# Kernel optimization log

Hardware: AMD Instinct MI355X
Metric: run time of the kernel (lower is better)

The kernel has to match this reference:

```python
import jax, jax.numpy as jnp
import numpy as np


def setup_inputs() -> dict:
    key = jax.random.key(0)
    k1, k2, k3, k4 = jax.random.split(key, 4)
    B, S, E, A = 4, 4096, 1024, 1024
    embedded = jax.random.normal(k1, (B, S, E), dtype=jnp.float32)
    # nn.Linear(E, A, bias=False) weights, stored as [E, A] so y = x @ W
    Wk = jax.random.normal(k2, (E, A), dtype=jnp.float32) * (E ** -0.5)
    Wq = jax.random.normal(k3, (E, A), dtype=jnp.float32) * (E ** -0.5)
    Wv = jax.random.normal(k4, (E, A), dtype=jnp.float32) * (E ** -0.5)
    return {"embedded": embedded, "Wk": Wk, "Wq": Wq, "Wv": Wv}


def reference(embedded, Wk, Wq, Wv):
    # K, Q, V projections: [B, S, A]
    K = embedded @ Wk
    Q = embedded @ Wq
    V = embedded @ Wv
    A = K.shape[-1]
    S = embedded.shape[1]
    # causal scores [B, S, S]
    scores = jnp.einsum("bqa,bka->bqk", Q, K) / jnp.sqrt(jnp.float32(A))
    causal = jnp.tril(jnp.ones((S, S), dtype=bool))
    scores = jnp.where(causal, scores, -jnp.inf)
    probs = jax.nn.softmax(scores, axis=-1)
    out = jnp.einsum("bqk,bka->bqa", probs, V)
    # torch.round(out, decimals=4)
    return jnp.round(out, 4)
```

## Files before the change

kernel.cpp:

```cpp
#include <hip/hip_runtime.h>
#include <hip/hip_fp16.h>

typedef __attribute__((ext_vector_type(4))) float f32x4;
typedef __attribute__((ext_vector_type(8))) short s16x8;
typedef __attribute__((ext_vector_type(4))) short s16x4;
typedef unsigned short u16;
typedef unsigned int u32;

__device__ __forceinline__ u16 f2bf(float f) {
    union { float f; unsigned u; } x; x.f = f;
    return (u16)((x.u + 0x7fffu + ((x.u >> 16) & 1u)) >> 16);
}

__device__ __forceinline__ void ld16(const void* g, void* l) {
    __builtin_amdgcn_global_load_lds(
        (const __attribute__((address_space(1))) unsigned int*)g,
        (__attribute__((address_space(3))) unsigned int*)l, 16, 0, 0);
}

__device__ __forceinline__ void kstep64(const u16* gA, const u16* gB, const u16* gC,
                                        long lda, long ldb,
                                        u16* sA, u16* sB,
                                        int wm, int wn, int lm, int lg,
                                        f32x4 acc0[4][4], f32x4 acc1[4][4])
{
    const int t = threadIdx.x;
    __syncthreads();
#pragma unroll
    for (int p = 0; p < 4; p++) {
        ld16(gA + (long)p * 32 * lda, sA + p * 2048 + t * 8);
        ld16(gB + (long)p * 32 * ldb, sB + p * 2048 + t * 8);
        ld16(gC + (long)p * 32 * ldb, sB + 8192 + p * 2048 + t * 8);
    }
    __syncthreads();

#pragma unroll
    for (int s = 0; s < 2; s++) {
        s16x8 af[4], bf[4], cf[4];
        const int co = (((s * 4 + lg) ^ (lm & 7)) << 3);
#pragma unroll
        for (int i = 0; i < 4; i++) {
            af[i] = *(const s16x8*)&sA[(wm + i * 16 + lm) * 64 + co];
            bf[i] = *(const s16x8*)&sB[(wn + i * 16 + lm) * 64 + co];
            cf[i] = *(const s16x8*)&sB[8192 + (wn + i * 16 + lm) * 64 + co];
        }
#pragma unroll
        for (int i = 0; i < 4; i++)
#pragma unroll
            for (int j = 0; j < 4; j++) {
                acc0[i][j] = __builtin_amdgcn_mfma_f32_16x16x32_bf16(af[i], bf[j], acc0[i][j], 0, 0, 0);
                acc1[i][j] = __builtin_amdgcn_mfma_f32_16x16x32_bf16(af[i], cf[j], acc1[i][j], 0, 0, 0);
            }
    }
}

__device__ __forceinline__ void gemm_core64(const u16* A, long lda,
                                            const u16* B0, const u16* B1, long ldb,
                                            int m0, int kEnd,
                                            f32x4 acc0[4][4], f32x4 acc1[4][4],
                                            u16* sA, u16* sB)
{
    const int t    = threadIdx.x;
    const int lane = t & 63;
    const int wave = t >> 6;
    const int wm   = (wave & 1) << 6;
    const int wn   = (wave >> 1) << 6;
    const int lm   = lane & 15;
    const int lg   = lane >> 4;
    const int sr   = t >> 3;
    const int sc   = (((t & 7) ^ ((t >> 3) & 7)) << 3);
    const u16* gA0 = A + (long)(m0 + sr) * lda + sc;
    const u16* gB0 = B0 + (long)sr * ldb + sc;
    const u16* gC0 = B1 + (long)sr * ldb + sc;

    for (int k0 = 0; k0 < kEnd; k0 += 64)
        kstep64(gA0 + k0, gB0 + k0, gC0 + k0, lda, ldb,
                sA, sB, wm, wn, lm, lg, acc0, acc1);
}

__global__ void convert_x(const float* __restrict__ X, u16* __restrict__ Xb) {
    long idx = ((long)blockIdx.x * 256 + threadIdx.x) * 4;
    f32x4 v = *(const f32x4*)&X[idx];
    s16x4 o;
    o.x = (short)f2bf(v.x); o.y = (short)f2bf(v.y);
    o.z = (short)f2bf(v.z); o.w = (short)f2bf(v.w);
    *(s16x4*)&Xb[idx] = o;
}

__global__ void convert_w(const float* __restrict__ Wk, const float* __restrict__ Wq,
                          const float* __restrict__ Wv,
                          u16* __restrict__ Wkt, u16* __restrict__ Wqt, u16* __restrict__ Wvt) {
    const float* W; u16* O;
    if (blockIdx.y == 0)      { W = Wk; O = Wkt; }
    else if (blockIdx.y == 1) { W = Wq; O = Wqt; }
    else                      { W = Wv; O = Wvt; }
    __shared__ u16 tile[64][65];
    int k0 = (blockIdx.x >> 4) << 6, n0 = (blockIdx.x & 15) << 6;
    int t = threadIdx.x;
    int rr = t >> 4, cc = (t & 15) << 2;
#pragma unroll
    for (int i = 0; i < 4; i++) {
        int row = rr + i * 16;
        f32x4 v = *(const f32x4*)&W[(long)(k0 + row) * 1024 + n0 + cc];
        tile[row][cc + 0] = f2bf(v.x); tile[row][cc + 1] = f2bf(v.y);
        tile[row][cc + 2] = f2bf(v.z); tile[row][cc + 3] = f2bf(v.w);
    }
    __syncthreads();
#pragma unroll
    for (int i = 0; i < 4; i++) {
        int row = rr + i * 16;
        s16x4 pk;
        pk.x = (short)tile[cc + 0][row]; pk.y = (short)tile[cc + 1][row];
        pk.z = (short)tile[cc + 2][row]; pk.w = (short)tile[cc + 3][row];
        *(s16x4*)&O[(long)(n0 + row) * 1024 + k0 + cc] = pk;
    }
}

__device__ __forceinline__ void stage_half64(const u16* gbase, u16* lbase,
                                             int kt, int h, int t) {
    const u16* g = gbase + (long)(h * 128) * 1024 + kt * 64;
    u16* l = lbase + h * 8192 + t * 8;
    ld16(g, l);
    ld16(g + 64 * 1024, l + 4096);
}

__device__ __forceinline__ void read_A8(const u16* sA, int arow, int ih,
                                        int co0, int co1, s16x8 af[4][2]) {
#pragma unroll
    for (int i = 0; i < 4; i++) {
        af[i][0] = *(const s16x8*)&sA[(arow + (ih * 4 + i) * 16) * 64 + co0];
        af[i][1] = *(const s16x8*)&sA[(arow + (ih * 4 + i) * 16) * 64 + co1];
    }
}

__device__ __forceinline__ void read_B4(const u16* sB, int brow, int jp,
                                        int co0, int co1, s16x8 bf[4][2]) {
#pragma unroll
    for (int j = 2 * jp; j < 2 * jp + 2; j++) {
        bf[j][0] = *(const s16x8*)&sB[(brow + j * 16) * 64 + co0];
        bf[j][1] = *(const s16x8*)&sB[(brow + j * 16) * 64 + co1];
    }
}

__device__ __forceinline__ void mfma16q(f32x4 acc[8][4], const s16x8 af[4][2],
                                        const s16x8 bf[4][2], int ih, int jh) {
    __builtin_amdgcn_s_setprio(1);
#pragma unroll
    for (int s = 0; s < 2; s++)
#pragma unroll
        for (int i = 0; i < 4; i++)
#pragma unroll
            for (int j = 0; j < 2; j++)
                acc[ih * 4 + i][jh * 2 + j] = __builtin_amdgcn_mfma_f32_16x16x32_bf16(
                    af[i][s], bf[jh * 2 + j][s], acc[ih * 4 + i][jh * 2 + j], 0, 0, 0);
    __builtin_amdgcn_s_setprio(0);
}

#define ABAR() asm volatile("s_barrier" ::: "memory")

__global__ __launch_bounds__(512, 2) void proj_all8(const u16* __restrict__ X,
                                                    const u16* __restrict__ Wqt,
                                                    const u16* __restrict__ Wkt,
                                                    const u16* __restrict__ Wvt,
                                                    u16* __restrict__ Qb,
                                                    u16* __restrict__ Kb,
                                                    u16* __restrict__ Vt) {
    __shared__ u16 lds[65536];
    const int bx  = ((blockIdx.x & 7) * 96) + (blockIdx.x >> 3);
    const int z   = bx >> 8;
    const int rem = bx & 255;
    const int m0  = (rem >> 2) << 8;
    const int n0  = (rem & 3) << 8;
    const u16* Wt = (z == 0) ? Wqt : (z == 1) ? Wkt : Wvt;

    const int t  = threadIdx.x;
    const int sr = t >> 3;
    const int sc = ((t & 7) ^ (sr & 7)) << 3;
    const u16* Ast = X  + (long)(m0 + sr) * 1024 + sc;
    const u16* Bst = Wt + (long)(n0 + sr) * 1024 + sc;
    u16* sA0 = lds;
    u16* sA1 = lds + 16384;
    u16* sB0 = lds + 32768;
    u16* sB1 = lds + 49152;

    const int lane = t & 63, w = t >> 6;
    const int wr = w >> 2, wc = w & 3;
    const int lm = lane & 15, lg = lane >> 4;
    const int arow = wr * 128 + lm;
    const int brow = wc * 64 + lm;
    const int co0 = ((lg) ^ (lm & 7)) << 3;
    const int co1 = ((4 + lg) ^ (lm & 7)) << 3;

    f32x4 acc[8][4] = {};
    s16x8 af[4][2], bf[4][2];

    stage_half64(Bst, sB0, 0, 0, t); stage_half64(Bst, sB0, 0, 1, t);
    stage_half64(Ast, sA0, 0, 0, t); stage_half64(Ast, sA0, 0, 1, t);
    stage_half64(Bst, sB1, 1, 0, t); stage_half64(Bst, sB1, 1, 1, t);
    asm volatile("s_waitcnt vmcnt(4)" ::: "memory");
    ABAR();

#pragma unroll 1
    for (int it = 0; it < 8; it++) {
        const int  tO   = 2 * it + 1;
        const bool more = (it < 7);
        read_A8(sA0, arow, 0, co0, co1, af);
        read_B4(sB0, brow, 0, co0, co1, bf);
        stage_half64(Ast, sA1, tO, 0, t);
        mfma16q(acc, af, bf, 0, 0);
        ABAR();
        read_B4(sB0, brow, 1, co0, co1, bf);
        stage_half64(Ast, sA1, tO, 1, t);
        mfma16q(acc, af, bf, 0, 1);
        ABAR();
        read_A8(sA0, arow, 1, co0, co1, af);
        if (more) stage_half64(Bst, sB0, tO + 1, 0, t);
        mfma16q(acc, af, bf, 1, 0);
        ABAR();
        if (more) stage_half64(Bst, sB0, tO + 1, 1, t);
        mfma16q(acc, af, bf, 1, 1);
        if (more) asm volatile("s_waitcnt vmcnt(4)" ::: "memory");
        else      asm volatile("s_waitcnt vmcnt(0)" ::: "memory");
        ABAR();
        read_A8(sA1, arow, 0, co0, co1, af);
        read_B4(sB1, brow, 0, co0, co1, bf);
        if (more) stage_half64(Ast, sA0, tO + 1, 0, t);
        mfma16q(acc, af, bf, 0, 0);
        ABAR();
        read_B4(sB1, brow, 1, co0, co1, bf);
        if (more) stage_half64(Ast, sA0, tO + 1, 1, t);
        mfma16q(acc, af, bf, 0, 1);
        ABAR();
        read_A8(sA1, arow, 1, co0, co1, af);
        if (more) stage_half64(Bst, sB1, tO + 2, 0, t);
        mfma16q(acc, af, bf, 1, 0);
        ABAR();
        if (more) stage_half64(Bst, sB1, tO + 2, 1, t);
        mfma16q(acc, af, bf, 1, 1);
        if (more) asm volatile("s_waitcnt vmcnt(4)" ::: "memory");
        ABAR();
    }

    if (z < 2) {
        u16* O = (z == 0) ? Qb : Kb;
#pragma unroll
        for (int i = 0; i < 8; i++)
#pragma unroll
            for (int j = 0; j < 4; j++)
#pragma unroll
                for (int r = 0; r < 4; r++) {
                    int row = m0 + wr * 128 + i * 16 + lg * 4 + r;
                    int col = n0 + wc * 64 + j * 16 + lm;
                    O[(long)row * 1024 + col] = f2bf(acc[i][j][r]);
                }
    } else {
#pragma unroll
        for (int i = 0; i < 8; i++)
#pragma unroll
            for (int j = 0; j < 4; j++) {
                int row0 = m0 + wr * 128 + i * 16 + lg * 4;
                int col  = n0 + wc * 64 + j * 16 + lm;
                int b = row0 >> 12, s = row0 & 4095;
                s16x4 p0;
                p0.x = (short)f2bf(acc[i][j][0]); p0.y = (short)f2bf(acc[i][j][1]);
                p0.z = (short)f2bf(acc[i][j][2]); p0.w = (short)f2bf(acc[i][j][3]);
                *(s16x4*)&Vt[(long)b * 4194304 + (long)col * 4096 + s] = p0;
            }
    }
}

__global__ __launch_bounds__(256, 2) void sgemm_causal(const u16* __restrict__ Q,
                                                       const u16* __restrict__ K,
                                                       u16* __restrict__ S,
                                                       float* __restrict__ l) {
    __shared__ u16 sA[8192], sB[16384];
    int b  = blockIdx.x / 272;
    int tt = blockIdx.x % 272;
    int it = (int)(2.0f * sqrtf((float)tt + 1.0f)) - 1;
    if (it > 31) it = 31;
    if (it < 0) it = 0;
    while (it < 31 && (((it + 2) * (it + 2)) >> 2) <= tt) ++it;
    while (it > 0 && (((it + 1) * (it + 1)) >> 2) > tt) --it;
    int jp  = tt - (((it + 1) * (it + 1)) >> 2);
    int jt0 = jp * 2, jt1 = jt0 + 1;
    bool valid1 = (jt1 <= it);

    const u16* A  = Q + (long)b * 4194304;
    const u16* Kp = K + (long)b * 4194304;
    f32x4 acc0[4][4] = {}, acc1[4][4] = {};
    gemm_core64(A, 1024, Kp + (long)jt0 * 131072, Kp + (long)jt1 * 131072, 1024,
                it * 128, 1024, acc0, acc1, sA, sB);

    long tribase = (long)(b * 528 + ((it * (it + 1)) >> 1));
    u16* Sp0 = S + (tribase + jt0) * 16384;
    u16* Sp1 = S + (tribase + jt1) * 16384;
    int lane = threadIdx.x & 63, wave = threadIdx.x >> 6;
    int wm = (wave & 1) << 6, wn = (wave >> 1) << 6, lm = lane & 15, lg = lane >> 4;
    const float LOG2E = 1.44269504088896f;

    float rs[4][4];
#pragma unroll
    for (int i = 0; i < 4; i++)
#pragma unroll
        for (int r = 0; r < 4; r++) rs[i][r] = 0.0f;

#pragma unroll
    for (int i = 0; i < 4; i++)
#pragma unroll
        for (int j = 0; j < 4; j++)
#pragma unroll
            for (int r = 0; r < 4; r++) {
                int ri = wm + i * 16 + lg * 4 + r;
                int cj = wn + j * 16 + lm;
                int gi = it * 128 + ri;
                float p0 = (jt0 * 128 + cj > gi) ? 0.0f
                         : exp2f((acc0[i][j][r] * 0.03125f - 16.0f) * LOG2E);
                Sp0[ri * 128 + cj] = f2bf(p0);
                rs[i][r] += p0;
                if (valid1) {
                    float p1 = (jt1 * 128 + cj > gi) ? 0.0f
                             : exp2f((acc1[i][j][r] * 0.03125f - 16.0f) * LOG2E);
                    Sp1[ri * 128 + cj] = f2bf(p1);
                    rs[i][r] += p1;
                }
            }

#pragma unroll
    for (int i = 0; i < 4; i++)
#pragma unroll
        for (int r = 0; r < 4; r++) {
            float s = rs[i][r];
            s += __shfl_xor(s, 1, 64);
            s += __shfl_xor(s, 2, 64);
            s += __shfl_xor(s, 4, 64);
            s += __shfl_xor(s, 8, 64);
            if (lm == 0)
                atomicAdd(&l[b * 4096 + it * 128 + wm + i * 16 + lg * 4 + r], s);
        }
}

__global__ __launch_bounds__(256, 2) void pv_gemm(const u16* __restrict__ P,
                                                  const u16* __restrict__ Vt,
                                                  const float* __restrict__ l,
                                                  float* __restrict__ Out) {
    __shared__ u16 sA[8192], sB[16384];
    int g  = blockIdx.x;
    int it = (g < 256) ? (31 - (g >> 4)) : ((g - 256) >> 4);
    int rem = g & 15;
    int b   = rem >> 2;
    int atp = rem & 3;

    const int t    = threadIdx.x;
    const int lane = t & 63;
    const int wave = t >> 6;
    const int wm   = (wave & 1) << 6;
    const int wn   = (wave >> 1) << 6;
    const int lm   = lane & 15;
    const int lg   = lane >> 4;
    const int sr   = t >> 3;
    const int sc   = (((t & 7) ^ ((t >> 3) & 7)) << 3);

    const u16* Pbase = P + (long)(b * 528 + ((it * (it + 1)) >> 1)) * 16384;
    const u16* gA0 = Pbase + sr * 128 + sc;
    const u16* gB0 = Vt + (long)b * 4194304 + (long)(atp * 256 + sr) * 4096 + sc;
    const u16* gC0 = gB0 + (long)128 * 4096;

    f32x4 acc0[4][4] = {}, acc1[4][4] = {};
    for (int jt = 0; jt <= it; jt++) {
        long aoff = (long)jt * 16384;
        long boff = (long)jt * 128;
#pragma unroll
        for (int kk = 0; kk < 128; kk += 64)
            kstep64(gA0 + aoff + kk, gB0 + boff + kk, gC0 + boff + kk,
                    128, 4096, sA, sB, wm, wn, lm, lg, acc0, acc1);
    }

#pragma unroll
    for (int i = 0; i < 4; i++)
#pragma unroll
        for (int r = 0; r < 4; r++) {
            int gi = it * 128 + wm + i * 16 + lg * 4 + r;
            float scale = 1.0f / l[b * 4096 + gi];
#pragma unroll
            for (int j = 0; j < 4; j++) {
                int ga = atp * 256 + wn + j * 16 + lm;
                float* o = &Out[((long)b * 4096 + gi) * 1024 + ga];
                o[0]   = acc0[i][j][r] * scale;
                o[128] = acc1[i][j][r] * scale;
            }
        }
}

extern "C" void kernel_launch(void* const* d_in, const int* in_sizes, int n_in,
                              void* d_out, int out_size, void* d_ws, size_t ws_size,
                              hipStream_t stream) {
    const float* X  = (const float*)d_in[0];
    const float* Wk = (const float*)d_in[1];
    const float* Wq = (const float*)d_in[2];
    const float* Wv = (const float*)d_in[3];
    float* Out = (float*)d_out;

    char* w = (char*)d_ws;
    u16*   Qb   = (u16*)(w);
    u16*   Kb   = (u16*)(w + 33554432);
    u16*   Vt   = (u16*)(w + 67108864);
    float* l    = (float*)(w + 100663296);
    u16*   Xb   = (u16*)(w + 100728832);
    u16*   Wqt  = (u16*)(w + 134283264);
    u16*   Wkt  = (u16*)(w + 136380416);
    u16*   Wvt  = (u16*)(w + 138477568);
    u16*   S    = (u16*)(w + 100728832);

    hipMemsetAsync(l, 0, 65536, stream);
    convert_x<<<16384, 256, 0, stream>>>(X, Xb);
    convert_w<<<dim3(256, 3), 256, 0, stream>>>(Wk, Wq, Wv, Wkt, Wqt, Wvt);
    proj_all8<<<768, 512, 0, stream>>>(Xb, Wqt, Wkt, Wvt, Qb, Kb, Vt);
    sgemm_causal<<<1088, 256, 0, stream>>>(Qb, Kb, S, l);
    pv_gemm<<<512, 256, 0, stream>>>(S, Vt, l, Out);
}
```

Baseline: 421.2 us.

## Move causal QK^T scores GEMM onto shared 256x256 eight-phase pipelined core

Pulls the projection GEMM's 256x256, 512-thread, double-buffered eight-phase pipeline into a shared helper and uses it for the causal score kernel, which previously used 128x256 tiles over a 64-wide k-step core. Blocks now cover 256x256 lower-triangular tile pairs (136 per batch) with an XCD-aware block remap. Each wave writes its own 128x128 sub-tile of S and skips the one fully masked sub-tile on the diagonal. Larger tiles should improve operand reuse and MFMA efficiency. In exchange, diagonal tiles do wasted MFMA work on the masked quadrant and there are fewer blocks in flight.

```diff
diff --git a/kernel.cpp b/kernel.cpp
--- a/kernel.cpp
+++ b/kernel.cpp
@@ -52,30 +52,6 @@
                 acc1[i][j] = __builtin_amdgcn_mfma_f32_16x16x32_bf16(af[i], cf[j], acc1[i][j], 0, 0, 0);
             }
     }
-}
-
-__device__ __forceinline__ void gemm_core64(const u16* A, long lda,
-                                            const u16* B0, const u16* B1, long ldb,
-                                            int m0, int kEnd,
-                                            f32x4 acc0[4][4], f32x4 acc1[4][4],
-                                            u16* sA, u16* sB)
-{
-    const int t    = threadIdx.x;
-    const int lane = t & 63;
-    const int wave = t >> 6;
-    const int wm   = (wave & 1) << 6;
-    const int wn   = (wave >> 1) << 6;
-    const int lm   = lane & 15;
-    const int lg   = lane >> 4;
-    const int sr   = t >> 3;
-    const int sc   = (((t & 7) ^ ((t >> 3) & 7)) << 3);
-    const u16* gA0 = A + (long)(m0 + sr) * lda + sc;
-    const u16* gB0 = B0 + (long)sr * ldb + sc;
-    const u16* gC0 = B1 + (long)sr * ldb + sc;
-
-    for (int k0 = 0; k0 < kEnd; k0 += 64)
-        kstep64(gA0 + k0, gB0 + k0, gC0 + k0, lda, ldb,
-                sA, sB, wm, wn, lm, lg, acc0, acc1);
 }
 
 __global__ void convert_x(const float* __restrict__ X, u16* __restrict__ Xb) {
@@ -157,6 +133,69 @@
 }
 
 #define ABAR() asm volatile("s_barrier" ::: "memory")
+
+__device__ __forceinline__ void gemm256_8ph(const u16* Abase, const u16* Bbase,
+                                            u16* lds, int t,
+                                            int arow, int brow, int co0, int co1,
+                                            f32x4 acc[8][4]) {
+    const int sr = t >> 3;
+    const int sc = ((t & 7) ^ (sr & 7)) << 3;
+    const u16* Ast = Abase + (long)sr * 1024 + sc;
+    const u16* Bst = Bbase + (long)sr * 1024 + sc;
+    u16* sA0 = lds;
+    u16* sA1 = lds + 16384;
+    u16* sB0 = lds + 32768;
+    u16* sB1 = lds + 49152;
+
+    s16x8 af[4][2], bf[4][2];
+
+    stage_half64(Bst, sB0, 0, 0, t); stage_half64(Bst, sB0, 0, 1, t);
+    stage_half64(Ast, sA0, 0, 0, t); stage_half64(Ast, sA0, 0, 1, t);
+    stage_half64(Bst, sB1, 1, 0, t); stage_half64(Bst, sB1, 1, 1, t);
+    asm volatile("s_waitcnt vmcnt(4)" ::: "memory");
+    ABAR();
+
+#pragma unroll 1
+    for (int it = 0; it < 8; it++) {
+        const int  tO   = 2 * it + 1;
+        const bool more = (it < 7);
+        read_A8(sA0, arow, 0, co0, co1, af);
+        read_B4(sB0, brow, 0, co0, co1, bf);
+        stage_half64(Ast, sA1, tO, 0, t);
+        mfma16q(acc, af, bf, 0, 0);
+        ABAR();
+        read_B4(sB0, brow, 1, co0, co1, bf);
+        stage_half64(Ast, sA1, tO, 1, t);
+        mfma16q(acc, af, bf, 0, 1);
+        ABAR();
+        read_A8(sA0, arow, 1, co0, co1, af);
+        if (more) stage_half64(Bst, sB0, tO + 1, 0, t);
+        mfma16q(acc, af, bf, 1, 0);
+        ABAR();
+        if (more) stage_half64(Bst, sB0, tO + 1, 1, t);
+        mfma16q(acc, af, bf, 1, 1);
+        if (more) asm volatile("s_waitcnt vmcnt(4)" ::: "memory");
+        else      asm volatile("s_waitcnt vmcnt(0)" ::: "memory");
+        ABAR();
+        read_A8(sA1, arow, 0, co0, co1, af);
+        read_B4(sB1, brow, 0, co0, co1, bf);
+        if (more) stage_half64(Ast, sA0, tO + 1, 0, t);
+        mfma16q(acc, af, bf, 0, 0);
+        ABAR();
+        read_B4(sB1, brow, 1, co0, co1, bf);
+        if (more) stage_half64(Ast, sA0, tO + 1, 1, t);
+        mfma16q(acc, af, bf, 0, 1);
+        ABAR();
+        read_A8(sA1, arow, 1, co0, co1, af);
+        if (more) stage_half64(Bst, sB1, tO + 2, 0, t);
+        mfma16q(acc, af, bf, 1, 0);
+        ABAR();
+        if (more) stage_half64(Bst, sB1, tO + 2, 1, t);
+        mfma16q(acc, af, bf, 1, 1);
+        if (more) asm volatile("s_waitcnt vmcnt(4)" ::: "memory");
+        ABAR();
+    }
+}
 
 __global__ __launch_bounds__(512, 2) void proj_all8(const u16* __restrict__ X,
                                                     const u16* __restrict__ Wqt,
@@ -173,16 +212,7 @@
     const int n0  = (rem & 3) << 8;
     const u16* Wt = (z == 0) ? Wqt : (z == 1) ? Wkt : Wvt;
 
-    const int t  = threadIdx.x;
-    const int sr = t >> 3;
-    const int sc = ((t & 7) ^ (sr & 7)) << 3;
-    const u16* Ast = X  + (long)(m0 + sr) * 1024 + sc;
-    const u16* Bst = Wt + (long)(n0 + sr) * 1024 + sc;
-    u16* sA0 = lds;
-    u16* sA1 = lds + 16384;
-    u16* sB0 = lds + 32768;
-    u16* sB1 = lds + 49152;
-
+    const int t    = threadIdx.x;
     const int lane = t & 63, w = t >> 6;
     const int wr = w >> 2, wc = w & 3;
     const int lm = lane & 15, lg = lane >> 4;
@@ -192,54 +222,8 @@
     const int co1 = ((4 + lg) ^ (lm & 7)) << 3;
 
     f32x4 acc[8][4] = {};
-    s16x8 af[4][2], bf[4][2];
-
-    stage_half64(Bst, sB0, 0, 0, t); stage_half64(Bst, sB0, 0, 1, t);
-    stage_half64(Ast, sA0, 0, 0, t); stage_half64(Ast, sA0, 0, 1, t);
-    stage_half64(Bst, sB1, 1, 0, t); stage_half64(Bst, sB1, 1, 1, t);
-    asm volatile("s_waitcnt vmcnt(4)" ::: "memory");
-    ABAR();
-
-#pragma unroll 1
-    for (int it = 0; it < 8; it++) {
-        const int  tO   = 2 * it + 1;
-        const bool more = (it < 7);
-        read_A8(sA0, arow, 0, co0, co1, af);
-        read_B4(sB0, brow, 0, co0, co1, bf);
-        stage_half64(Ast, sA1, tO, 0, t);
-        mfma16q(acc, af, bf, 0, 0);
-        ABAR();
-        read_B4(sB0, brow, 1, co0, co1, bf);
-        stage_half64(Ast, sA1, tO, 1, t);
-        mfma16q(acc, af, bf, 0, 1);
-        ABAR();
-        read_A8(sA0, arow, 1, co0, co1, af);
-        if (more) stage_half64(Bst, sB0, tO + 1, 0, t);
-        mfma16q(acc, af, bf, 1, 0);
-        ABAR();
-        if (more) stage_half64(Bst, sB0, tO + 1, 1, t);
-        mfma16q(acc, af, bf, 1, 1);
-        if (more) asm volatile("s_waitcnt vmcnt(4)" ::: "memory");
-        else      asm volatile("s_waitcnt vmcnt(0)" ::: "memory");
-        ABAR();
-        read_A8(sA1, arow, 0, co0, co1, af);
-        read_B4(sB1, brow, 0, co0, co1, bf);
-        if (more) stage_half64(Ast, sA0, tO + 1, 0, t);
-        mfma16q(acc, af, bf, 0, 0);
-        ABAR();
-        read_B4(sB1, brow, 1, co0, co1, bf);
-        if (more) stage_half64(Ast, sA0, tO + 1, 1, t);
-        mfma16q(acc, af, bf, 0, 1);
-        ABAR();
-        read_A8(sA1, arow, 1, co0, co1, af);
-        if (more) stage_half64(Bst, sB1, tO + 2, 0, t);
-        mfma16q(acc, af, bf, 1, 0);
-        ABAR();
-        if (more) stage_half64(Bst, sB1, tO + 2, 1, t);
-        mfma16q(acc, af, bf, 1, 1);
-        if (more) asm volatile("s_waitcnt vmcnt(4)" ::: "memory");
-        ABAR();
-    }
+    gemm256_8ph(X + (long)m0 * 1024, Wt + (long)n0 * 1024, lds, t,
+                arow, brow, co0, co1, acc);
 
     if (z < 2) {
         u16* O = (z == 0) ? Qb : Kb;
@@ -269,64 +253,73 @@
     }
 }
 
-__global__ __launch_bounds__(256, 2) void sgemm_causal(const u16* __restrict__ Q,
-                                                       const u16* __restrict__ K,
-                                                       u16* __restrict__ S,
-                                                       float* __restrict__ l) {
-    __shared__ u16 sA[8192], sB[16384];
-    int b  = blockIdx.x / 272;
-    int tt = blockIdx.x % 272;
-    int it = (int)(2.0f * sqrtf((float)tt + 1.0f)) - 1;
-    if (it > 31) it = 31;
-    if (it < 0) it = 0;
-    while (it < 31 && (((it + 2) * (it + 2)) >> 2) <= tt) ++it;
-    while (it > 0 && (((it + 1) * (it + 1)) >> 2) > tt) --it;
-    int jp  = tt - (((it + 1) * (it + 1)) >> 2);
-    int jt0 = jp * 2, jt1 = jt0 + 1;
-    bool valid1 = (jt1 <= it);
-
-    const u16* A  = Q + (long)b * 4194304;
+__global__ __launch_bounds__(512, 2) void sgemm_causal8(const u16* __restrict__ Q,
+                                                        const u16* __restrict__ K,
+                                                        u16* __restrict__ S,
+                                                        float* __restrict__ l) {
+    __shared__ u16 lds[65536];
+    const int bx = ((blockIdx.x & 7) * 68) + (blockIdx.x >> 3);
+    const int b  = bx / 136;
+    const int tt = bx % 136;
+    int it2 = (int)((sqrtf(8.0f * (float)tt + 1.0f) - 1.0f) * 0.5f);
+    if (it2 > 15) it2 = 15;
+    if (it2 < 0) it2 = 0;
+    while (it2 < 15 && ((it2 + 1) * (it2 + 2)) / 2 <= tt) ++it2;
+    while (it2 > 0 && (it2 * (it2 + 1)) / 2 > tt) --it2;
+    const int jt2 = tt - (it2 * (it2 + 1)) / 2;
+
+    const int m0 = it2 << 8;
+    const int n0 = jt2 << 8;
+
+    const int t    = threadIdx.x;
+    const int lane = t & 63, w = t >> 6;
+    const int wr = w >> 2, wc = w & 3;
+    const int lm = lane & 15, lg = lane >> 4;
+    const int arow = wr * 128 + lm;
+    const int brow = wc * 64 + lm;
+    const int co0 = ((lg) ^ (lm & 7)) << 3;
+    const int co1 = ((4 + lg) ^ (lm & 7)) << 3;
+
+    const u16* Qp = Q + (long)b * 4194304;
     const u16* Kp = K + (long)b * 4194304;
-    f32x4 acc0[4][4] = {}, acc1[4][4] = {};
-    gemm_core64(A, 1024, Kp + (long)jt0 * 131072, Kp + (long)jt1 * 131072, 1024,
-                it * 128, 1024, acc0, acc1, sA, sB);
-
-    long tribase = (long)(b * 528 + ((it * (it + 1)) >> 1));
-    u16* Sp0 = S + (tribase + jt0) * 16384;
-    u16* Sp1 = S + (tribase + jt1) * 16384;
-    int lane = threadIdx.x & 63, wave = threadIdx.x >> 6;
-    int wm = (wave & 1) << 6, wn = (wave >> 1) << 6, lm = lane & 15, lg = lane >> 4;
+
+    f32x4 acc[8][4] = {};
+    gemm256_8ph(Qp + (long)m0 * 1024, Kp + (long)n0 * 1024, lds, t,
+                arow, brow, co0, co1, acc);
+
+    const int jtl = wc >> 1;
+    const int itg = 2 * it2 + wr;
+    const int jtg = 2 * jt2 + jtl;
+    const bool skip = (jt2 == it2) && (wr == 0) && (jtl == 1);
+    u16* Sp = S + ((long)(b * 528 + ((itg * (itg + 1)) >> 1) + jtg)) * 16384;
     const float LOG2E = 1.44269504088896f;
 
-    float rs[4][4];
-#pragma unroll
-    for (int i = 0; i < 4; i++)
+    float rs[8][4];
+#pragma unroll
+    for (int i = 0; i < 8; i++)
 #pragma unroll
         for (int r = 0; r < 4; r++) rs[i][r] = 0.0f;
 
-#pragma unroll
-    for (int i = 0; i < 4; i++)
-#pragma unroll
-        for (int j = 0; j < 4; j++)
-#pragma unroll
-            for (int r = 0; r < 4; r++) {
-                int ri = wm + i * 16 + lg * 4 + r;
-                int cj = wn + j * 16 + lm;
-                int gi = it * 128 + ri;
-                float p0 = (jt0 * 128 + cj > gi) ? 0.0f
-                         : exp2f((acc0[i][j][r] * 0.03125f - 16.0f) * LOG2E);
-                Sp0[ri * 128 + cj] = f2bf(p0);
-                rs[i][r] += p0;
-                if (valid1) {
-                    float p1 = (jt1 * 128 + cj > gi) ? 0.0f
-                             : exp2f((acc1[i][j][r] * 0.03125f - 16.0f) * LOG2E);
-                    Sp1[ri * 128 + cj] = f2bf(p1);
-                    rs[i][r] += p1;
+    if (!skip) {
+#pragma unroll
+        for (int i = 0; i < 8; i++)
+#pragma unroll
+            for (int j = 0; j < 4; j++)
+#pragma unroll
+                for (int r = 0; r < 4; r++) {
+                    int ri = i * 16 + lg * 4 + r;
+                    int cj = (wc & 1) * 64 + j * 16 + lm;
+                    int grow = m0 + wr * 128 + ri;
+                    int gcol = n0 + jtl * 128 + cj;
+                    float p = (gcol > grow) ? 0.0f
+                            : exp2f((acc[i][j][r] * 0.03125f - 16.0f) * LOG2E);
+                    Sp[ri * 128 + cj] = f2bf(p);
+                    rs[i][r] += p;
                 }
-            }
-
-#pragma unroll
-    for (int i = 0; i < 4; i++)
+    }
+
+#pragma unroll
+    for (int i = 0; i < 8; i++)
 #pragma unroll
         for (int r = 0; r < 4; r++) {
             float s = rs[i][r];
@@ -334,8 +327,8 @@
             s += __shfl_xor(s, 2, 64);
             s += __shfl_xor(s, 4, 64);
             s += __shfl_xor(s, 8, 64);
-            if (lm == 0)
-                atomicAdd(&l[b * 4096 + it * 128 + wm + i * 16 + lg * 4 + r], s);
+            if (lm == 0 && !skip)
+                atomicAdd(&l[b * 4096 + m0 + wr * 128 + i * 16 + lg * 4 + r], s);
         }
 }
 
@@ -415,6 +408,6 @@
     convert_x<<<16384, 256, 0, stream>>>(X, Xb);
     convert_w<<<dim3(256, 3), 256, 0, stream>>>(Wk, Wq, Wv, Wkt, Wqt, Wvt);
     proj_all8<<<768, 512, 0, stream>>>(Xb, Wqt, Wkt, Wvt, Qb, Kb, Vt);
-    sgemm_causal<<<1088, 256, 0, stream>>>(Qb, Kb, S, l);
+    sgemm_causal8<<<544, 512, 0, stream>>>(Qb, Kb, S, l);
     pv_gemm<<<512, 256, 0, stream>>>(S, Vt, l, Out);
 }
```

Measured after the change: 430.5 us. 1.02x slower.
